# Kernel optimization log

Measured on AMD Instinct MI355X. Metric: run time of the kernel, lower is better.

## Reference

```python
import jax, jax.numpy as jnp
import numpy as np

N_EMBD = 1024
N_HEAD = 16
B, T = 4, 2048


def setup_inputs() -> dict:
    key = jax.random.key(0)
    ks = jax.random.split(key, 9)
    s = 1.0 / np.sqrt(N_EMBD)
    def lin(k):
        kw, kb = jax.random.split(k)
        W = jax.random.uniform(kw, (N_EMBD, N_EMBD), jnp.float32, -s, s)
        b = jax.random.uniform(kb, (N_EMBD,), jnp.float32, -s, s)
        return W, b
    Wq, bq = lin(ks[0])
    Wk, bk = lin(ks[1])
    Wv, bv = lin(ks[2])
    Wc, bc = lin(ks[3])
    x = jax.random.normal(ks[4], (B, T, N_EMBD), jnp.float32)
    return {"x": x, "Wq": Wq, "bq": bq, "Wk": Wk, "bk": bk,
            "Wv": Wv, "bv": bv, "Wc": Wc, "bc": bc}


def reference(x, Wq, bq, Wk, bk, Wv, bv, Wc, bc):
    Bsz, Tlen, C = x.shape
    hd = C // N_HEAD  # head dim
    # projections (torch Linear: x @ W.T + b)
    q = x @ Wq.T + bq
    k = x @ Wk.T + bk
    v = x @ Wv.T + bv
    # [B, H, T, hd]
    q = q.reshape(Bsz, Tlen, N_HEAD, hd).transpose(0, 2, 1, 3)
    k = k.reshape(Bsz, Tlen, N_HEAD, hd).transpose(0, 2, 1, 3)
    v = v.reshape(Bsz, Tlen, N_HEAD, hd).transpose(0, 2, 1, 3)
    scale = 1.0 / np.sqrt(hd).astype(np.float32)
    att = jnp.einsum('bhqd,bhkd->bhqk', q, k) * scale  # [B,H,T,T]
    causal = jnp.tril(jnp.ones((Tlen, Tlen), dtype=bool))
    att = jnp.where(causal[None, None, :, :], att, -jnp.inf)
    att = jax.nn.softmax(att, axis=-1)
    y = jnp.einsum('bhqk,bhkd->bhqd', att, v)  # [B,H,T,hd]
    y = y.transpose(0, 2, 1, 3).reshape(Bsz, Tlen, C)
    return y @ Wc.T + bc
```

## Files before the change

### kernel.cpp

```cpp
#include <hip/hip_runtime.h>
#include <hip/hip_bf16.h>

typedef __bf16 bf16x8 __attribute__((ext_vector_type(8)));
typedef float f32x4 __attribute__((ext_vector_type(4)));
typedef unsigned short u16;
typedef u16 u16x8 __attribute__((ext_vector_type(8)));
typedef unsigned int u32;
typedef u32 u32x4 __attribute__((ext_vector_type(4)));

#define N_EMBD 1024
#define NH 16
#define HD 64
#define BZ 4
#define TZ 2048
#define QSCALE 0.18033688011f

template<bool B> struct BoolC { static constexpr bool value = B; };

__device__ __forceinline__ u16 f2bf(float f) {
    return __builtin_bit_cast(u16, (__bf16)f);
}

__device__ __forceinline__ void gload16(const void* g, void* l) {
    __builtin_amdgcn_global_load_lds(
        (const __attribute__((address_space(1))) void*)g,
        (__attribute__((address_space(3))) void*)l, 16, 0, 0);
}

__global__ void cvt_f32_bf16(const float* __restrict__ src, u16* __restrict__ dst,
                             int n4, float scale) {
    int i = blockIdx.x * blockDim.x + threadIdx.x;
    if (i < n4) {
        float4 f = ((const float4*)src)[i];
        ushort4 o;
        o.x = f2bf(f.x * scale); o.y = f2bf(f.y * scale);
        o.z = f2bf(f.z * scale); o.w = f2bf(f.w * scale);
        ((ushort4*)dst)[i] = o;
    }
}

template<int EPI>
__global__ __launch_bounds__(512, 2) void gemm_bt(
    const u16* __restrict__ A, const u16* __restrict__ Bm,
    const float* __restrict__ b0, const float* __restrict__ b1, const float* __restrict__ b2,
    void* __restrict__ Cout, int K) {
    __shared__ __align__(16) u16 Ash[2][2][8192];
    __shared__ __align__(16) u16 Bsh[2][2][8192];

    const int tid = threadIdx.x;
    const int lane = tid & 63, wid = tid >> 6;
    const int wm = wid >> 2, wn = wid & 3;
    const int m0 = blockIdx.x * 256, n0 = blockIdx.y * 256;
    const int r = lane & 15, g = lane >> 4;

    f32x4 acc[8][4] = {};

    const int p0 = tid >> 3;
    const int ci = tid & 7;
    const int cl = ci ^ (p0 & 7);
    const int trow = 2 * p0 + (cl >> 2);
    const int colb = (cl & 3) * 8;
    const u16* aS = A + (long)(m0 + trow) * K + colb;
    const u16* bS = Bm + (long)(n0 + trow) * K + colb;
    const long rowskip = (long)128 * K;
    const int ldst = tid * 8;

    auto STAGE_A = [&](int slot, int kh, int kt) {
        const u16* sp = aS + kt * 64 + kh * 32;
        gload16(sp, &Ash[slot][kh][ldst]);
        gload16(sp + rowskip, &Ash[slot][kh][4096 + ldst]);
    };
    auto STAGE_B = [&](int slot, int kh, int kt) {
        const u16* sp = bS + kt * 64 + kh * 32;
        gload16(sp, &Bsh[slot][kh][ldst]);
        gload16(sp + rowskip, &Bsh[slot][kh][4096 + ldst]);
    };

    const int xa = (((((r & 1) << 2) | g) ^ (r >> 1)) << 4);
    const int arow0 = wm * 64 + (r >> 1);
    const int brow0 = wn * 32 + (r >> 1);
    auto RD = [&](const u16* base, int prow) -> bf16x8 {
        return *(const bf16x8*)((const char*)base + prow * 128 + xa);
    };

    bf16x8 bfr[4];

#define PHASE(S, KH, QM, STG, ENDW)                                              \
    {                                                                            \
        bf16x8 af[4];                                                            \
        _Pragma("unroll")                                                        \
        for (int m = 0; m < 4; ++m)                                              \
            af[m] = RD(&Ash[S][KH][0], arow0 + QM * 32 + m * 8);                 \
        if (QM == 0) {                                                           \
            _Pragma("unroll")                                                    \
            for (int n = 0; n < 4; ++n)                                          \
                bfr[n] = RD(&Bsh[S][KH][0], brow0 + n * 8);                      \
        }                                                                        \
        STG;                                                                     \
        __builtin_amdgcn_s_barrier();                                            \
        asm volatile("s_waitcnt lgkmcnt(0)" ::: "memory");                       \
        __builtin_amdgcn_s_setprio(1);                                           \
        _Pragma("unroll")                                                        \
        for (int m = 0; m < 4; ++m)                                              \
            _Pragma("unroll")                                                    \
            for (int n = 0; n < 4; ++n)                                          \
                acc[QM * 4 + m][n] = __builtin_amdgcn_mfma_f32_16x16x32_bf16(    \
                    af[m], bfr[n], acc[QM * 4 + m][n], 0, 0, 0);                 \
        __builtin_amdgcn_s_setprio(0);                                           \
        if (ENDW) asm volatile("s_waitcnt vmcnt(8)" ::: "memory");               \
        asm volatile("" ::: "memory");                                           \
        __builtin_amdgcn_s_barrier();                                            \
        asm volatile("" ::: "memory");                                           \
    }

    STAGE_A(0, 0, 0); STAGE_B(0, 0, 0);
    STAGE_A(0, 1, 0); STAGE_B(0, 1, 0);
    STAGE_A(1, 0, 1); STAGE_B(1, 0, 1);
    asm volatile("s_waitcnt vmcnt(8)" ::: "memory");
    __builtin_amdgcn_s_barrier();
    asm volatile("" ::: "memory");

    const int nt = K >> 6;
    for (int tt = 0; tt < nt; tt += 2) {
        const int kt1 = tt + 1;
        const int kt2 = (tt + 2 < nt) ? tt + 2 : 0;
        const int kt3 = (tt + 3 < nt) ? tt + 3 : 0;
        PHASE(0, 0, 0, STAGE_A(1, 1, kt1), 0)
        PHASE(0, 0, 1, STAGE_B(1, 1, kt1), 1)
        PHASE(0, 1, 0, STAGE_A(0, 0, kt2), 0)
        PHASE(0, 1, 1, STAGE_B(0, 0, kt2), 1)
        PHASE(1, 0, 0, STAGE_A(0, 1, kt2), 0)
        PHASE(1, 0, 1, STAGE_B(0, 1, kt2), 1)
        PHASE(1, 1, 0, STAGE_A(1, 0, kt3), 0)
        PHASE(1, 1, 1, STAGE_B(1, 0, kt3), 1)
    }
#undef PHASE
    asm volatile("s_waitcnt vmcnt(0)" ::: "memory");

    const long planeSz = (long)BZ * NH * TZ * HD;
    if constexpr (EPI == 0) {
        const int proj = n0 >> 10;
        u16* outp = (u16*)Cout;
        if (proj == 2) {
            const int bi = (m0 + wm * 128) >> 11;
#pragma unroll
            for (int n = 0; n < 4; ++n) {
                const int rr = (n0 & 1023) + wn * 64 + n * 16 + r;
                const int h = rr >> 6, d = rr & 63;
                const float bias = b2[rr];
                u16* vcol = outp + 2 * planeSz + (((long)bi * NH + h) * HD + d) * TZ;
#pragma unroll
                for (int mf = 0; mf < 8; ++mf) {
                    const int t0 = (m0 + wm * 128 + mf * 16 + g * 4) & 2047;
                    ushort4 o;
                    o.x = f2bf(acc[mf][n][0] + bias);
                    o.y = f2bf(acc[mf][n][1] + bias);
                    o.z = f2bf(acc[mf][n][2] + bias);
                    o.w = f2bf(acc[mf][n][3] + bias);
                    *(ushort4*)(vcol + t0) = o;
                }
            }
        } else {
#pragma unroll
            for (int n = 0; n < 4; ++n) {
                const int rr = (n0 & 1023) + wn * 64 + n * 16 + r;
                const int h = rr >> 6, d = rr & 63;
                float bias = (proj == 0 ? b0 : b1)[rr];
                if (proj == 0) bias *= QSCALE;
                const long pbase = (long)proj * planeSz + d;
#pragma unroll
                for (int mf = 0; mf < 8; ++mf)
#pragma unroll
                    for (int reg = 0; reg < 4; ++reg) {
                        const int row = m0 + wm * 128 + mf * 16 + g * 4 + reg;
                        const int bi = row >> 11, t = row & 2047;
                        outp[pbase + ((long)bi * NH + h) * (TZ * HD) + (long)t * HD] =
                            f2bf(acc[mf][n][reg] + bias);
                    }
            }
        }
    } else {
        float* outp = (float*)Cout;
#pragma unroll
        for (int n = 0; n < 4; ++n) {
            const int col = n0 + wn * 64 + n * 16 + r;
            const float bias = b0[col];
#pragma unroll
            for (int mf = 0; mf < 8; ++mf)
#pragma unroll
                for (int reg = 0; reg < 4; ++reg) {
                    const int row = m0 + wm * 128 + mf * 16 + g * 4 + reg;
                    outp[(long)row * N_EMBD + col] = acc[mf][n][reg] + bias;
                }
        }
    }
}

__device__ __forceinline__ bf16x8 lds_swz8(const u16* base, int row, int colByte) {
    return *(const bf16x8*)((const char*)base + row * 128 + (colByte ^ ((row & 7) << 4)));
}

__global__ __launch_bounds__(256, 4) void attn_fwd(const u16* __restrict__ qkv, u16* __restrict__ yb) {
    const int i = blockIdx.x;
    const int xcd = i & 7, slot = i >> 3;
    const int bh = xcd + 8 * (slot & 7);
    const int pr = slot >> 3;
    const int b = bh >> 4, h = bh & 15;
    const int tid = threadIdx.x, lane = tid & 63, w = tid >> 6;
    const int r = lane & 15, g = lane >> 4;

    __shared__ __align__(16) u16 Ksh[2][64 * 64];
    __shared__ __align__(16) u16 Vsh[2][64 * 64];

    const long planeSz = (long)BZ * NH * TZ * HD;
    const long bhoff = ((long)b * NH + h) * (long)TZ * HD;
    const u16* qp = qkv + bhoff;
    const u16* kp = qkv + planeSz + bhoff;
    const u16* vTp = qkv + 2 * planeSz + bhoff;

    const int rr8 = tid >> 3, scb = tid & 7;

#pragma unroll 1
    for (int it = 0; it < 2; ++it) {
        const int qblk = it ? pr : (31 - pr);
        const int q0 = qblk * 64;
        const int nkt = qblk + 1;

        bf16x8 qf[2];
        {
            const int q = q0 + w * 16 + r;
#pragma unroll
            for (int ks = 0; ks < 2; ++ks)
                qf[ks] = *(const bf16x8*)(qp + (long)q * HD + ks * 32 + g * 8);
        }

        f32x4 yacc[4] = {};
        float mrun = -__builtin_inff(), lpart = 0.f;

#pragma unroll
        for (int h2 = 0; h2 < 2; ++h2) {
            const int kk = h2 * 32 + rr8;
            const int ss = (scb ^ (kk & 7)) * 8;
            gload16(kp + (long)kk * HD + ss, &Ksh[0][h2 * 2048 + tid * 8]);
            gload16(vTp + (long)kk * TZ + ss, &Vsh[0][h2 * 2048 + tid * 8]);
        }

        auto tile = [&](int kt, auto maskc) {
            constexpr bool MASK = decltype(maskc)::value;
            const int cur = kt & 1;
            const int k0 = kt * 64;
            if (kt + 1 < nkt) {
                const int k0n = k0 + 64;
#pragma unroll
                for (int h2 = 0; h2 < 2; ++h2) {
                    const int kk = h2 * 32 + rr8;
                    const int ss = (scb ^ (kk & 7)) * 8;
                    gload16(kp + (long)(k0n + kk) * HD + ss, &Ksh[cur ^ 1][h2 * 2048 + tid * 8]);
                    gload16(vTp + (long)kk * TZ + k0n + ss, &Vsh[cur ^ 1][h2 * 2048 + tid * 8]);
                }
                asm volatile("s_waitcnt vmcnt(4)" ::: "memory");
            } else {
                asm volatile("s_waitcnt vmcnt(0)" ::: "memory");
            }
            __builtin_amdgcn_s_barrier();
            asm volatile("" ::: "memory");

            f32x4 sac[4] = {};
#pragma unroll
            for (int ks = 0; ks < 2; ++ks) {
                bf16x8 kf[4];
#pragma unroll
                for (int nk = 0; nk < 4; ++nk)
                    kf[nk] = lds_swz8(Ksh[cur], nk * 16 + r, ks * 64 + g * 16);
                __builtin_amdgcn_s_setprio(1);
#pragma unroll
                for (int nk = 0; nk < 4; ++nk)
                    sac[nk] = __builtin_amdgcn_mfma_f32_16x16x32_bf16(kf[nk], qf[ks], sac[nk], 0, 0, 0);
                __builtin_amdgcn_s_setprio(0);
            }

            if constexpr (MASK) {
                const int q = q0 + w * 16 + r;
#pragma unroll
                for (int nk = 0; nk < 4; ++nk)
#pragma unroll
                    for (int reg = 0; reg < 4; ++reg) {
                        const int k = k0 + nk * 16 + g * 4 + reg;
                        sac[nk][reg] = (k > q) ? -__builtin_inff() : sac[nk][reg];
                    }
            }
            float pmax;
            {
                float t0 = fmaxf(fmaxf(sac[0][0], sac[0][1]), fmaxf(sac[0][2], sac[0][3]));
                float t1 = fmaxf(fmaxf(sac[1][0], sac[1][1]), fmaxf(sac[1][2], sac[1][3]));
                float t2 = fmaxf(fmaxf(sac[2][0], sac[2][1]), fmaxf(sac[2][2], sac[2][3]));
                float t3 = fmaxf(fmaxf(sac[3][0], sac[3][1]), fmaxf(sac[3][2], sac[3][3]));
                pmax = fmaxf(fmaxf(t0, t1), fmaxf(t2, t3));
            }
            if (__any(pmax > mrun + 8.0f)) {
                float mx = pmax;
                mx = fmaxf(mx, __shfl_xor(mx, 16));
                mx = fmaxf(mx, __shfl_xor(mx, 32));
                const float mnew = fmaxf(mrun, mx);
                const float corr = __builtin_amdgcn_exp2f(mrun - mnew);
                lpart *= corr;
#pragma unroll
                for (int nd = 0; nd < 4; ++nd)
                    yacc[nd] *= corr;
                mrun = mnew;
            }
            float rs[4];
#pragma unroll
            for (int nk = 0; nk < 4; ++nk) {
                float p0 = __builtin_amdgcn_exp2f(sac[nk][0] - mrun);
                float p1 = __builtin_amdgcn_exp2f(sac[nk][1] - mrun);
                float p2 = __builtin_amdgcn_exp2f(sac[nk][2] - mrun);
                float p3 = __builtin_amdgcn_exp2f(sac[nk][3] - mrun);
                sac[nk][0] = p0; sac[nk][1] = p1;
                sac[nk][2] = p2; sac[nk][3] = p3;
                rs[nk] = (p0 + p1) + (p2 + p3);
            }
            lpart += (rs[0] + rs[1]) + (rs[2] + rs[3]);

            u32 wv[4][2];
#pragma unroll
            for (int nk = 0; nk < 4; ++nk)
#pragma unroll
                for (int j2 = 0; j2 < 2; ++j2)
                    asm("v_cvt_pk_bf16_f32 %0, %1, %2"
                        : "=v"(wv[nk][j2])
                        : "v"(sac[nk][2 * j2]), "v"(sac[nk][2 * j2 + 1]));
            u32 pw[2][4];
#pragma unroll
            for (int ks = 0; ks < 2; ++ks) {
                u32 a0 = wv[2 * ks][0], b0 = wv[2 * ks + 1][0];
                u32 a1 = wv[2 * ks][1], b1 = wv[2 * ks + 1][1];
                asm("v_permlane32_swap_b32 %0, %1" : "+v"(a0), "+v"(b0));
                asm("v_permlane32_swap_b32 %0, %1" : "+v"(a1), "+v"(b1));
                asm("v_permlane16_swap_b32 %0, %1" : "+v"(a0), "+v"(b0));
                asm("v_permlane16_swap_b32 %0, %1" : "+v"(a1), "+v"(b1));
                pw[ks][0] = a0; pw[ks][1] = a1;
                pw[ks][2] = b0; pw[ks][3] = b1;
            }

#pragma unroll
            for (int ks = 0; ks < 2; ++ks) {
                bf16x8 vf[4];
#pragma unroll
                for (int nd = 0; nd < 4; ++nd)
                    vf[nd] = lds_swz8(Vsh[cur], nd * 16 + r, ks * 64 + g * 16);
                const u32x4 pwv = { pw[ks][0], pw[ks][1], pw[ks][2], pw[ks][3] };
                const bf16x8 pb = __builtin_bit_cast(bf16x8, pwv);
                __builtin_amdgcn_s_setprio(1);
#pragma unroll
                for (int nd = 0; nd < 4; ++nd)
                    yacc[nd] = __builtin_amdgcn_mfma_f32_16x16x32_bf16(vf[nd], pb, yacc[nd], 0, 0, 0);
                __builtin_amdgcn_s_setprio(0);
            }

            asm volatile("" ::: "memory");
            __builtin_amdgcn_s_barrier();
            asm volatile("" ::: "memory");
        };

        for (int kt = 0; kt < nkt - 1; ++kt) tile(kt, BoolC<false>{});
        tile(nkt - 1, BoolC<true>{});

        {
            float l = lpart;
            l += __shfl_xor(l, 16);
            l += __shfl_xor(l, 32);
            const float inv = 1.f / l;
            const int q = q0 + w * 16 + r;
            u16* orow = yb + ((long)b * TZ + q) * N_EMBD + h * HD;
#pragma unroll
            for (int nd = 0; nd < 4; ++nd) {
                ushort4 o;
                o.x = f2bf(yacc[nd][0] * inv);
                o.y = f2bf(yacc[nd][1] * inv);
                o.z = f2bf(yacc[nd][2] * inv);
                o.w = f2bf(yacc[nd][3] * inv);
                *(ushort4*)(orow + nd * 16 + g * 4) = o;
            }
        }
    }
}

extern "C" void kernel_launch(void* const* d_in, const int* in_sizes, int n_in,
                              void* d_out, int out_size, void* d_ws, size_t ws_size,
                              hipStream_t stream) {
    const float* x  = (const float*)d_in[0];
    const float* Wq = (const float*)d_in[1];
    const float* bq = (const float*)d_in[2];
    const float* Wk = (const float*)d_in[3];
    const float* bk = (const float*)d_in[4];
    const float* Wv = (const float*)d_in[5];
    const float* bv = (const float*)d_in[6];
    const float* Wc = (const float*)d_in[7];
    const float* bc = (const float*)d_in[8];

    char* ws = (char*)d_ws;
    u16* xb   = (u16*)(ws);
    u16* wqkv = (u16*)(ws + 16777216);
    u16* wcb  = (u16*)(ws + 23068672);
    u16* qkv  = (u16*)(ws + 25165824);
    u16* yb   = (u16*)(ws + 75497472);

    cvt_f32_bf16<<<8192, 256, 0, stream>>>(x, xb, 2097152, 1.0f);
    cvt_f32_bf16<<<1024, 256, 0, stream>>>(Wq, wqkv, 262144, QSCALE);
    cvt_f32_bf16<<<1024, 256, 0, stream>>>(Wk, wqkv + 1048576, 262144, 1.0f);
    cvt_f32_bf16<<<1024, 256, 0, stream>>>(Wv, wqkv + 2097152, 262144, 1.0f);
    cvt_f32_bf16<<<1024, 256, 0, stream>>>(Wc, wcb, 262144, 1.0f);

    gemm_bt<0><<<dim3(32, 12), 512, 0, stream>>>(xb, wqkv, bq, bk, bv, (void*)qkv, 1024);

    attn_fwd<<<1024, 256, 0, stream>>>(qkv, yb);

    gemm_bt<1><<<dim3(32, 4), 512, 0, stream>>>(yb, wcb, bc, nullptr, nullptr, d_out, 1024);
}
```

Measured before the change: 185.4 us.

## Split GEMM K across wave pairs with 256x128 tiles and triple-buffered LDS

The bf16 GEMM changes its output tile from 256x256 to 256x128 and splits the K loop across pairs of waves. Each pair of waves computes the same output fragment on alternate 32-wide K halves, and the partial sums are reduced through LDS before the epilogue. LDS is reorganised into a 3-stage ring buffer (about 144 KB) that prefetches two K-tiles ahead, and both GEMM launches double their grid in the N dimension. The goal is more blocks for CU occupancy and better latency hiding. The cost is an extra LDS reduction and at most one resident block per CU because of the larger shared-memory footprint.

After: 438.1 us. 136% more time.

```diff
diff --git a/kernel.cpp b/kernel.cpp
--- a/kernel.cpp
+++ b/kernel.cpp
@@ -44,13 +44,15 @@
     const u16* __restrict__ A, const u16* __restrict__ Bm,
     const float* __restrict__ b0, const float* __restrict__ b1, const float* __restrict__ b2,
     void* __restrict__ Cout, int K) {
-    __shared__ __align__(16) u16 Ash[2][2][8192];
-    __shared__ __align__(16) u16 Bsh[2][2][8192];
+    __shared__ __align__(16) char SH[147456];
+    u16* Ash = (u16*)SH;
+    u16* Bsh = (u16*)(SH + 98304);
 
     const int tid = threadIdx.x;
     const int lane = tid & 63, wid = tid >> 6;
-    const int wm = wid >> 2, wn = wid & 3;
-    const int m0 = blockIdx.x * 256, n0 = blockIdx.y * 256;
+    const int sk = wid & 1, ww = wid >> 1;
+    const int wm = ww >> 1, wn = ww & 1;
+    const int m0 = blockIdx.x * 256, n0 = blockIdx.y * 128;
     const int r = lane & 15, g = lane >> 4;
 
     f32x4 acc[8][4] = {};
@@ -65,15 +67,14 @@
     const long rowskip = (long)128 * K;
     const int ldst = tid * 8;
 
-    auto STAGE_A = [&](int slot, int kh, int kt) {
-        const u16* sp = aS + kt * 64 + kh * 32;
-        gload16(sp, &Ash[slot][kh][ldst]);
-        gload16(sp + rowskip, &Ash[slot][kh][4096 + ldst]);
+    auto STG_A = [&](int buf, int kh, int kq) {
+        const u16* sp = aS + kq * 32;
+        u16* d = Ash + buf * 16384 + kh * 8192 + ldst;
+        gload16(sp, d);
+        gload16(sp + rowskip, d + 4096);
     };
-    auto STAGE_B = [&](int slot, int kh, int kt) {
-        const u16* sp = bS + kt * 64 + kh * 32;
-        gload16(sp, &Bsh[slot][kh][ldst]);
-        gload16(sp + rowskip, &Bsh[slot][kh][4096 + ldst]);
+    auto STG_B = [&](int buf, int kh, int kq) {
+        gload16(bS + kq * 32, Bsh + buf * 8192 + kh * 4096 + ldst);
     };
 
     const int xa = (((((r & 1) << 2) | g) ^ (r >> 1)) << 4);
@@ -83,18 +84,20 @@
         return *(const bf16x8*)((const char*)base + prow * 128 + xa);
     };
 
-    bf16x8 bfr[4];
-
-#define PHASE(S, KH, QM, STG, ENDW)                                              \
+    bf16x8 bf_[4];
+
+#define PH(BUF, MH, STG, WAITV)                                                  \
     {                                                                            \
         bf16x8 af[4];                                                            \
+        const u16* abase = Ash + (BUF) * 16384 + sk * 8192;                      \
         _Pragma("unroll")                                                        \
         for (int m = 0; m < 4; ++m)                                              \
-            af[m] = RD(&Ash[S][KH][0], arow0 + QM * 32 + m * 8);                 \
-        if (QM == 0) {                                                           \
+            af[m] = RD(abase, arow0 + MH * 32 + m * 8);                          \
+        if (MH == 0) {                                                           \
+            const u16* bbase = Bsh + (BUF) * 8192 + sk * 4096;                   \
             _Pragma("unroll")                                                    \
             for (int n = 0; n < 4; ++n)                                          \
-                bfr[n] = RD(&Bsh[S][KH][0], brow0 + n * 8);                      \
+                bf_[n] = RD(bbase, brow0 + n * 8);                               \
         }                                                                        \
         STG;                                                                     \
         __builtin_amdgcn_s_barrier();                                            \
@@ -104,38 +107,53 @@
         for (int m = 0; m < 4; ++m)                                              \
             _Pragma("unroll")                                                    \
             for (int n = 0; n < 4; ++n)                                          \
-                acc[QM * 4 + m][n] = __builtin_amdgcn_mfma_f32_16x16x32_bf16(    \
-                    af[m], bfr[n], acc[QM * 4 + m][n], 0, 0, 0);                 \
+                acc[MH * 4 + m][n] = __builtin_amdgcn_mfma_f32_16x16x32_bf16(    \
+                    af[m], bf_[n], acc[MH * 4 + m][n], 0, 0, 0);                 \
         __builtin_amdgcn_s_setprio(0);                                           \
-        if (ENDW) asm volatile("s_waitcnt vmcnt(8)" ::: "memory");               \
+        WAITV;                                                                   \
         asm volatile("" ::: "memory");                                           \
         __builtin_amdgcn_s_barrier();                                            \
         asm volatile("" ::: "memory");                                           \
     }
 
-    STAGE_A(0, 0, 0); STAGE_B(0, 0, 0);
-    STAGE_A(0, 1, 0); STAGE_B(0, 1, 0);
-    STAGE_A(1, 0, 1); STAGE_B(1, 0, 1);
-    asm volatile("s_waitcnt vmcnt(8)" ::: "memory");
+    STG_A(0, 0, 0); STG_A(0, 1, 1); STG_B(0, 0, 0); STG_B(0, 1, 1);
+    STG_A(1, 0, 2); STG_A(1, 1, 3); STG_B(1, 0, 2); STG_B(1, 1, 3);
+    asm volatile("s_waitcnt vmcnt(6)" ::: "memory");
     __builtin_amdgcn_s_barrier();
     asm volatile("" ::: "memory");
 
     const int nt = K >> 6;
-    for (int tt = 0; tt < nt; tt += 2) {
-        const int kt1 = tt + 1;
-        const int kt2 = (tt + 2 < nt) ? tt + 2 : 0;
-        const int kt3 = (tt + 3 < nt) ? tt + 3 : 0;
-        PHASE(0, 0, 0, STAGE_A(1, 1, kt1), 0)
-        PHASE(0, 0, 1, STAGE_B(1, 1, kt1), 1)
-        PHASE(0, 1, 0, STAGE_A(0, 0, kt2), 0)
-        PHASE(0, 1, 1, STAGE_B(0, 0, kt2), 1)
-        PHASE(1, 0, 0, STAGE_A(0, 1, kt2), 0)
-        PHASE(1, 0, 1, STAGE_B(0, 1, kt2), 1)
-        PHASE(1, 1, 0, STAGE_A(1, 0, kt3), 0)
-        PHASE(1, 1, 1, STAGE_B(1, 0, kt3), 1)
-    }
-#undef PHASE
-    asm volatile("s_waitcnt vmcnt(0)" ::: "memory");
+    for (int t = 0; t < nt; ++t) {
+        const int cur = t % 3;
+        const int nxt = (t + 2) % 3;
+        const bool pf = (t + 2) < nt;
+        const int kq = (t + 2) * 2;
+        if (pf) {
+            PH(cur, 0, { STG_A(nxt, 0, kq); STG_B(nxt, 0, kq); }, )
+            PH(cur, 1, { STG_A(nxt, 1, kq + 1); STG_B(nxt, 1, kq + 1); },
+               asm volatile("s_waitcnt vmcnt(6)" ::: "memory");)
+        } else {
+            PH(cur, 0, , )
+            PH(cur, 1, , asm volatile("s_waitcnt vmcnt(0)" ::: "memory");)
+        }
+    }
+#undef PH
+
+    {
+        f32x4* red = (f32x4*)SH;
+        if (sk == 1) {
+#pragma unroll
+            for (int i = 0; i < 32; ++i)
+                red[ww * 2048 + i * 64 + lane] = acc[i >> 2][i & 3];
+        }
+        __syncthreads();
+        if (sk == 0) {
+#pragma unroll
+            for (int i = 0; i < 32; ++i)
+                acc[i >> 2][i & 3] += red[ww * 2048 + i * 64 + lane];
+        }
+    }
+    if (sk != 0) return;
 
     const long planeSz = (long)BZ * NH * TZ * HD;
     if constexpr (EPI == 0) {
@@ -412,9 +430,9 @@
     cvt_f32_bf16<<<1024, 256, 0, stream>>>(Wv, wqkv + 2097152, 262144, 1.0f);
     cvt_f32_bf16<<<1024, 256, 0, stream>>>(Wc, wcb, 262144, 1.0f);
 
-    gemm_bt<0><<<dim3(32, 12), 512, 0, stream>>>(xb, wqkv, bq, bk, bv, (void*)qkv, 1024);
+    gemm_bt<0><<<dim3(32, 24), 512, 0, stream>>>(xb, wqkv, bq, bk, bv, (void*)qkv, 1024);
 
     attn_fwd<<<1024, 256, 0, stream>>>(qkv, yb);
 
-    gemm_bt<1><<<dim3(32, 4), 512, 0, stream>>>(yb, wcb, bc, nullptr, nullptr, d_out, 1024);
-}
+    gemm_bt<1><<<dim3(32, 8), 512, 0, stream>>>(yb, wcb, bc, nullptr, nullptr, d_out, 1024);
+}
```
